# Optimization experiments

Measured on AMD Instinct MI355X. Metric: run time of the kernel, lower is better.

The kernel has to match this reference:

```python
import jax, jax.numpy as jnp
import numpy as np

NG, NC, FG, FC, D = 8192, 4096, 512, 256, 64
ALPHA = 0.2          # leaky_relu negative slope
NEG = -9.0e15        # mask fill value from the torch code


def _leaky(x):
    return jnp.where(x >= 0, x, ALPHA * x)


def _relation(h_src, h_dst, a, adj):
    # additive GAT score: e[i,j] = leaky(h_src[i]@a[:D] + h_dst[j]@a[D:])
    s1 = h_src @ a[:D]            # [Ns]
    s2 = h_dst @ a[D:]            # [Nd]
    e = _leaky(s1[:, None] + s2[None, :])          # [Ns, Nd]
    att = jax.nn.softmax(jnp.where(adj > 0, e, NEG), axis=1)
    return att @ h_dst            # [Ns, D]


def setup_inputs() -> dict:
    key = jax.random.key(0)
    ks = jax.random.split(key, 14)
    sc = 0.05
    return {
        "gene_x": jax.random.normal(ks[0], (NG, FG), jnp.float32),
        "cell_x": jax.random.normal(ks[1], (NC, FC), jnp.float32),
        "W_g": jax.random.normal(ks[2], (FG, D), jnp.float32) * sc,
        "W_c": jax.random.normal(ks[3], (FC, D), jnp.float32) * sc,
        "a_gg": jax.random.normal(ks[4], (2 * D,), jnp.float32) * sc,
        "a_gc": jax.random.normal(ks[5], (2 * D,), jnp.float32) * sc,
        "a_cc": jax.random.normal(ks[6], (2 * D,), jnp.float32) * sc,
        "a_cg": jax.random.normal(ks[7], (2 * D,), jnp.float32) * sc,
        "Wgate_g": jax.random.normal(ks[8], (D, 1), jnp.float32) * sc,
        "bgate_g": jnp.full((1,), -2.0, jnp.float32),
        "Wgate_c": jax.random.normal(ks[9], (D, 1), jnp.float32) * sc,
        "bgate_c": jnp.full((1,), -2.0, jnp.float32),
        "gene_adj": jax.random.randint(ks[10], (NG, NG), 0, 2, jnp.int32),
        "cell_adj": jax.random.randint(ks[11], (NC, NC), 0, 2, jnp.int32),
        "gene_cell_adj": jax.random.randint(ks[12], (NG, NC), 0, 2, jnp.int32),
    }


def reference(gene_x, cell_x, W_g, W_c, a_gg, a_gc, a_cc, a_cg,
              Wgate_g, bgate_g, Wgate_c, bgate_c,
              gene_adj, cell_adj, gene_cell_adj):
    gene_h = gene_x @ W_g                              # [NG, D]
    cell_h = cell_x @ W_c                              # [NC, D]

    gene_from_gene = _relation(gene_h, gene_h, a_gg, gene_adj)
    gene_from_cell = _relation(gene_h, cell_h, a_gc, gene_cell_adj)
    cell_from_cell = _relation(cell_h, cell_h, a_cc, cell_adj)
    cell_from_gene = _relation(cell_h, gene_h, a_cg, gene_cell_adj.T)

    gamma_g = jax.nn.sigmoid(gene_h @ Wgate_g + bgate_g)   # [NG, 1]
    gamma_c = jax.nn.sigmoid(cell_h @ Wgate_c + bgate_c)   # [NC, 1]

    gene_out = _leaky(gene_h + gene_from_gene + gamma_g * gene_from_cell)
    cell_out = _leaky(cell_h + cell_from_cell + gamma_c * cell_from_gene)
    return gene_out, cell_out
```

## Files before the change

### kernel.cpp

```cpp
#include <hip/hip_runtime.h>

#define NG 8192
#define NC 4096
#define FG 512
#define FC 256
#define ALPHA 0.2f

typedef float f32x4 __attribute__((ext_vector_type(4)));
typedef short bf16x8 __attribute__((ext_vector_type(8)));

static __device__ __forceinline__ float leakyf(float x) { return fmaxf(x, ALPHA * x); }

static __device__ __forceinline__ unsigned short f2bf(float f) {
    unsigned u = __builtin_bit_cast(unsigned, f);
    u += 0x7fffu + ((u >> 16) & 1u);
    return (unsigned short)(u >> 16);
}

static __device__ __forceinline__ float wred(float v) {
#pragma unroll
    for (int m = 1; m < 64; m <<= 1) v += __shfl_xor(v, m, 64);
    return v;
}

__global__ __launch_bounds__(256) void pack_all(
    const int* __restrict__ gene_adj, const int* __restrict__ cell_adj,
    const int* __restrict__ gc_adj,
    unsigned char* __restrict__ bmGG, unsigned char* __restrict__ bmCC,
    unsigned char* __restrict__ bmGC)
{
    const int wave = threadIdx.x >> 6, lane = threadIdx.x & 63;
    const int r = blockIdx.x * 4 + wave;
    const int* row; unsigned char* brow; int C;
    if (r < NG)           { row = gene_adj + (size_t)r * NG;              brow = bmGG + (size_t)r * (NG >> 3);              C = NG; }
    else if (r < NG + NC) { int rr = r - NG;      row = cell_adj + (size_t)rr * NC; brow = bmCC + (size_t)rr * (NC >> 3); C = NC; }
    else                  { int rr = r - NG - NC; row = gc_adj   + (size_t)rr * NC; brow = bmGC + (size_t)rr * (NC >> 3); C = NC; }
    for (int j = lane * 8; j < C; j += 512) {
        int4 a0 = *(const int4*)(row + j);
        int4 a1 = *(const int4*)(row + j + 4);
        unsigned b = (unsigned)(a0.x > 0)        | ((unsigned)(a0.y > 0) << 1)
                   | ((unsigned)(a0.z > 0) << 2) | ((unsigned)(a0.w > 0) << 3)
                   | ((unsigned)(a1.x > 0) << 4) | ((unsigned)(a1.y > 0) << 5)
                   | ((unsigned)(a1.z > 0) << 6) | ((unsigned)(a1.w > 0) << 7);
        brow[j >> 3] = (unsigned char)b;
    }
}

__global__ __launch_bounds__(256) void proj_kernel(
    const float* __restrict__ x, const float* __restrict__ W, int K, int N,
    float* __restrict__ h, unsigned short* __restrict__ hT,
    const float* __restrict__ aA, const float* __restrict__ aB,
    const float* __restrict__ aC, const float* __restrict__ aD,
    const float* __restrict__ aG, const float* __restrict__ bG,
    float* __restrict__ sA, float* __restrict__ sB, float* __restrict__ sC,
    float* __restrict__ sD, float* __restrict__ gam)
{
    const int wave = threadIdx.x >> 6, lane = threadIdx.x & 63;
    const int r0 = blockIdx.x * 16 + wave * 4;
    const float* xr = x + (size_t)r0 * K;
    float acc0 = 0.f, acc1 = 0.f, acc2 = 0.f, acc3 = 0.f;
    for (int k = 0; k < K; k += 4) {
        float4 x0 = *(const float4*)(xr + k);
        float4 x1 = *(const float4*)(xr + K + k);
        float4 x2 = *(const float4*)(xr + 2 * (size_t)K + k);
        float4 x3 = *(const float4*)(xr + 3 * (size_t)K + k);
        float w0 = W[(k + 0) * 64 + lane];
        float w1 = W[(k + 1) * 64 + lane];
        float w2 = W[(k + 2) * 64 + lane];
        float w3 = W[(k + 3) * 64 + lane];
        acc0 += x0.x * w0 + x0.y * w1 + x0.z * w2 + x0.w * w3;
        acc1 += x1.x * w0 + x1.y * w1 + x1.z * w2 + x1.w * w3;
        acc2 += x2.x * w0 + x2.y * w1 + x2.z * w2 + x2.w * w3;
        acc3 += x3.x * w0 + x3.y * w1 + x3.z * w2 + x3.w * w3;
    }
    float accs[4] = {acc0, acc1, acc2, acc3};
    unsigned short hb[4];
#pragma unroll
    for (int t = 0; t < 4; t++) {
        h[(size_t)(r0 + t) * 64 + lane] = accs[t];
        hb[t] = f2bf(accs[t]);
    }
    *(ushort4*)&hT[(size_t)lane * N + r0] = make_ushort4(hb[0], hb[1], hb[2], hb[3]);

    const float cA = aA[lane], cB = aB[lane], cC = aC[lane], cD = aD[lane], cG = aG[lane];
    const float bias = bG[0];
#pragma unroll
    for (int t = 0; t < 4; t++) {
        float vA = wred(accs[t] * cA);
        float vB = wred(accs[t] * cB);
        float vC = wred(accs[t] * cC);
        float vD = wred(accs[t] * cD);
        float vG = wred(accs[t] * cG);
        if (lane == 0) {
            sA[r0 + t] = vA; sB[r0 + t] = vB; sC[r0 + t] = vC; sD[r0 + t] = vD;
            gam[r0 + t] = 1.f / (1.f + __expf(-(vG + bias)));
        }
    }
}

static __device__ __forceinline__ void rel_row_body(
    unsigned short* hbuf,
    const unsigned char* __restrict__ bm, int bm_ld,
    const float* __restrict__ s1, const float* __restrict__ s2,
    const unsigned short* __restrict__ hT, int Nd,
    float* __restrict__ num, float* __restrict__ lsum, int Ns, int JS,
    int strip, int p)
{
    const int wave = threadIdx.x >> 6, lane = threadIdx.x & 63;
    const int m = lane & 15, kp = lane >> 4;
    const int jlen = Nd / JS, jbase = p * jlen;
    const int i_row = strip * 64 + wave * 16 + m;
    const float s1v = s1[i_row];
    const unsigned char* bmrow = bm + (size_t)i_row * bm_ld;
    f32x4 acc0 = {0.f, 0.f, 0.f, 0.f}, acc1 = acc0, acc2 = acc0, acc3 = acc0;
    float lacc = 0.f;

    for (int jc = jbase; jc < jbase + jlen; jc += 256) {
        uint4 q0 = *(const uint4*)(bmrow + (jc >> 3));
        uint4 q1 = *(const uint4*)(bmrow + (jc >> 3) + 16);
        for (int idx = threadIdx.x; idx < 2048; idx += 256) {
            int c = idx >> 5, off = (idx & 31) * 8;
            *(int4*)&hbuf[c * 264 + off] = *(const int4*)&hT[(size_t)c * Nd + jc + off];
        }
        __syncthreads();
        unsigned words[8] = {q0.x, q0.y, q0.z, q0.w, q1.x, q1.y, q1.z, q1.w};
#pragma unroll
        for (int g = 0; g < 8; ++g) {
            const int jg = jc + g * 32 + kp * 8;
            float4 sa = *(const float4*)&s2[jg];
            float4 sb = *(const float4*)&s2[jg + 4];
            unsigned byte = (words[g] >> (kp * 8)) & 0xffu;
            const int lb = g * 32 + kp * 8;
            bf16x8 b0 = *(const bf16x8*)&hbuf[(0 * 16 + m) * 264 + lb];
            bf16x8 b1 = *(const bf16x8*)&hbuf[(1 * 16 + m) * 264 + lb];
            bf16x8 b2 = *(const bf16x8*)&hbuf[(2 * 16 + m) * 264 + lb];
            bf16x8 b3 = *(const bf16x8*)&hbuf[(3 * 16 + m) * 264 + lb];
            float s2v[8] = {sa.x, sa.y, sa.z, sa.w, sb.x, sb.y, sb.z, sb.w};
            bf16x8 af;
#pragma unroll
            for (int t = 0; t < 8; t++) {
                float e = s1v + s2v[t];
                float w = ((byte >> t) & 1u) ? __expf(leakyf(e)) : 0.f;
                lacc += w;
                af[t] = (short)f2bf(w);
            }
            acc0 = __builtin_amdgcn_mfma_f32_16x16x32_bf16(af, b0, acc0, 0, 0, 0);
            acc1 = __builtin_amdgcn_mfma_f32_16x16x32_bf16(af, b1, acc1, 0, 0, 0);
            acc2 = __builtin_amdgcn_mfma_f32_16x16x32_bf16(af, b2, acc2, 0, 0, 0);
            acc3 = __builtin_amdgcn_mfma_f32_16x16x32_bf16(af, b3, acc3, 0, 0, 0);
        }
        __syncthreads();
    }
    const int orow0 = strip * 64 + wave * 16 + kp * 4;
#pragma unroll
    for (int r = 0; r < 4; r++) {
        size_t base = ((size_t)p * Ns + orow0 + r) * 64;
        num[base + m]      = acc0[r];
        num[base + 16 + m] = acc1[r];
        num[base + 32 + m] = acc2[r];
        num[base + 48 + m] = acc3[r];
    }
    lacc += __shfl_xor(lacc, 16, 64);
    lacc += __shfl_xor(lacc, 32, 64);
    if (kp == 0) lsum[(size_t)p * Ns + strip * 64 + wave * 16 + m] = lacc;
}

static __device__ __forceinline__ void rel_col_body(
    unsigned short* hbuf,
    unsigned char* bmb,
    const unsigned char* __restrict__ bm, int bm_ld,
    const float* __restrict__ s1, const float* __restrict__ s2,
    const unsigned short* __restrict__ hT, int Nd,
    float* __restrict__ num, float* __restrict__ lsum, int Ns, int JS,
    int strip, int p)
{
    const int wave = threadIdx.x >> 6, lane = threadIdx.x & 63;
    const int m = lane & 15, kp = lane >> 4;
    const int jlen = Nd / JS, jbase = p * jlen;
    const int i0 = strip * 64;
    const float s1v = s1[i0 + wave * 16 + m];
    f32x4 acc0 = {0.f, 0.f, 0.f, 0.f}, acc1 = acc0, acc2 = acc0, acc3 = acc0;
    float lacc = 0.f;
    const int bidx = wave * 2 + (m >> 3);
    const int bbit = m & 7;

    for (int jc = jbase; jc < jbase + jlen; jc += 128) {
        if (threadIdx.x < 128)
            *(unsigned long long*)&bmb[threadIdx.x * 8] =
                *(const unsigned long long*)&bm[(size_t)(jc + threadIdx.x) * bm_ld + (i0 >> 3)];
        for (int idx = threadIdx.x; idx < 1024; idx += 256) {
            int c = idx >> 4, off = (idx & 15) * 8;
            *(int4*)&hbuf[c * 136 + off] = *(const int4*)&hT[(size_t)c * Nd + jc + off];
        }
        __syncthreads();
#pragma unroll
        for (int g = 0; g < 4; ++g) {
            const int jg = jc + g * 32 + kp * 8;
            float4 sa = *(const float4*)&s2[jg];
            float4 sb = *(const float4*)&s2[jg + 4];
            const int jl = g * 32 + kp * 8;
            bf16x8 b0 = *(const bf16x8*)&hbuf[(0 * 16 + m) * 136 + jl];
            bf16x8 b1 = *(const bf16x8*)&hbuf[(1 * 16 + m) * 136 + jl];
            bf16x8 b2 = *(const bf16x8*)&hbuf[(2 * 16 + m) * 136 + jl];
            bf16x8 b3 = *(const bf16x8*)&hbuf[(3 * 16 + m) * 136 + jl];
            float s2v[8] = {sa.x, sa.y, sa.z, sa.w, sb.x, sb.y, sb.z, sb.w};
            bf16x8 af;
#pragma unroll
            for (int t = 0; t < 8; t++) {
                unsigned byte = bmb[(jl + t) * 8 + bidx];
                float e = s1v + s2v[t];
                float w = ((byte >> bbit) & 1u) ? __expf(leakyf(e)) : 0.f;
                lacc += w;
                af[t] = (short)f2bf(w);
            }
            acc0 = __builtin_amdgcn_mfma_f32_16x16x32_bf16(af, b0, acc0, 0, 0, 0);
            acc1 = __builtin_amdgcn_mfma_f32_16x16x32_bf16(af, b1, acc1, 0, 0, 0);
            acc2 = __builtin_amdgcn_mfma_f32_16x16x32_bf16(af, b2, acc2, 0, 0, 0);
            acc3 = __builtin_amdgcn_mfma_f32_16x16x32_bf16(af, b3, acc3, 0, 0, 0);
        }
        __syncthreads();
    }
    const int orow0 = strip * 64 + wave * 16 + kp * 4;
#pragma unroll
    for (int r = 0; r < 4; r++) {
        size_t base = ((size_t)p * Ns + orow0 + r) * 64;
        num[base + m]      = acc0[r];
        num[base + 16 + m] = acc1[r];
        num[base + 32 + m] = acc2[r];
        num[base + 48 + m] = acc3[r];
    }
    lacc += __shfl_xor(lacc, 16, 64);
    lacc += __shfl_xor(lacc, 32, 64);
    if (kp == 0) lsum[(size_t)p * Ns + strip * 64 + wave * 16 + m] = lacc;
}

__global__ __launch_bounds__(256, 4) void rel_fused(
    const unsigned char* __restrict__ bmGG, const unsigned char* __restrict__ bmCC,
    const unsigned char* __restrict__ bmGC,
    const float* __restrict__ s1gg, const float* __restrict__ s2gg,
    const float* __restrict__ s1cc, const float* __restrict__ s2cc,
    const float* __restrict__ s1gc, const float* __restrict__ s2gc,
    const float* __restrict__ s1cg, const float* __restrict__ s2cg,
    const unsigned short* __restrict__ gene_hT, const unsigned short* __restrict__ cell_hT,
    float* __restrict__ numGG, float* __restrict__ lGG,
    float* __restrict__ numCC, float* __restrict__ lCC,
    float* __restrict__ numGC, float* __restrict__ lGC,
    float* __restrict__ numCG, float* __restrict__ lCG)
{
    __shared__ __align__(16) char smem[64 * 264 * 2];
    const int b = blockIdx.x, rel = b >> 9, w = b & 511;
    if (rel == 0) {
        rel_row_body((unsigned short*)smem, bmGG, NG / 8, s1gg, s2gg, gene_hT, NG,
                     numGG, lGG, NG, 4, w >> 2, w & 3);
    } else if (rel == 1) {
        rel_row_body((unsigned short*)smem, bmCC, NC / 8, s1cc, s2cc, cell_hT, NC,
                     numCC, lCC, NC, 8, w >> 3, w & 7);
    } else if (rel == 2) {
        rel_row_body((unsigned short*)smem, bmGC, NC / 8, s1gc, s2gc, cell_hT, NC,
                     numGC, lGC, NG, 4, w >> 2, w & 3);
    } else {
        rel_col_body((unsigned short*)smem, (unsigned char*)(smem + 64 * 136 * 2),
                     bmGC, NC / 8, s1cg, s2cg, gene_hT, NG,
                     numCG, lCG, NC, 8, w >> 3, w & 7);
    }
}

__global__ __launch_bounds__(256) void combine_final(
    const float* __restrict__ numS, const float* __restrict__ lS, int JSS,
    const float* __restrict__ numX, const float* __restrict__ lX, int JSX,
    int Ns, const float* __restrict__ h, const float* __restrict__ gam,
    float* __restrict__ out)
{
    int idx = blockIdx.x * 256 + threadIdx.x;
    int i = idx >> 6, c = idx & 63;
    float nS = 0.f, dS = 0.f, nX = 0.f, dX = 0.f;
    for (int p = 0; p < JSS; p++) {
        nS += numS[((size_t)p * Ns + i) * 64 + c];
        dS += lS[(size_t)p * Ns + i];
    }
    for (int p = 0; p < JSX; p++) {
        nX += numX[((size_t)p * Ns + i) * 64 + c];
        dX += lX[(size_t)p * Ns + i];
    }
    float v = h[idx] + nS / dS + gam[i] * (nX / dX);
    out[idx] = leakyf(v);
}

extern "C" void kernel_launch(void* const* d_in, const int* in_sizes, int n_in,
                              void* d_out, int out_size, void* d_ws, size_t ws_size,
                              hipStream_t stream)
{
    const float* gene_x = (const float*)d_in[0];
    const float* cell_x = (const float*)d_in[1];
    const float* W_g    = (const float*)d_in[2];
    const float* W_c    = (const float*)d_in[3];
    const float* a_gg   = (const float*)d_in[4];
    const float* a_gc   = (const float*)d_in[5];
    const float* a_cc   = (const float*)d_in[6];
    const float* a_cg   = (const float*)d_in[7];
    const float* Wgg    = (const float*)d_in[8];
    const float* bgg    = (const float*)d_in[9];
    const float* Wgc    = (const float*)d_in[10];
    const float* bgc    = (const float*)d_in[11];
    const int* gene_adj = (const int*)d_in[12];
    const int* cell_adj = (const int*)d_in[13];
    const int* gc_adj   = (const int*)d_in[14];

    size_t off = 0;
    char* wsb = (char*)d_ws;
    auto alloc = [&](size_t bytes) -> void* {
        void* p = wsb + off;
        off += (bytes + 255) & ~(size_t)255;
        return p;
    };
    const int JS_GG = 4, JS_CC = 8, JS_GC = 4, JS_CG = 8;

    float* gene_h = (float*)alloc((size_t)NG * 64 * 4);
    float* cell_h = (float*)alloc((size_t)NC * 64 * 4);
    unsigned short* gene_hT = (unsigned short*)alloc((size_t)NG * 64 * 2);
    unsigned short* cell_hT = (unsigned short*)alloc((size_t)NC * 64 * 2);
    unsigned char* bmGG = (unsigned char*)alloc((size_t)NG * (NG / 8));
    unsigned char* bmCC = (unsigned char*)alloc((size_t)NC * (NC / 8));
    unsigned char* bmGC = (unsigned char*)alloc((size_t)NG * (NC / 8));
    float* s1gg = (float*)alloc(NG * 4);
    float* s2gg = (float*)alloc(NG * 4);
    float* s1gc = (float*)alloc(NG * 4);
    float* s2cg = (float*)alloc(NG * 4);
    float* gamg = (float*)alloc(NG * 4);
    float* s1cc = (float*)alloc(NC * 4);
    float* s2cc = (float*)alloc(NC * 4);
    float* s2gc = (float*)alloc(NC * 4);
    float* s1cg = (float*)alloc(NC * 4);
    float* gamc = (float*)alloc(NC * 4);
    float* numGG = (float*)alloc((size_t)NG * 64 * JS_GG * 4);
    float* lGG   = (float*)alloc((size_t)NG * JS_GG * 4);
    float* numGC = (float*)alloc((size_t)NG * 64 * JS_GC * 4);
    float* lGC   = (float*)alloc((size_t)NG * JS_GC * 4);
    float* numCC = (float*)alloc((size_t)NC * 64 * JS_CC * 4);
    float* lCC   = (float*)alloc((size_t)NC * JS_CC * 4);
    float* numCG = (float*)alloc((size_t)NC * 64 * JS_CG * 4);
    float* lCG   = (float*)alloc((size_t)NC * JS_CG * 4);

    float* out_gene = (float*)d_out;
    float* out_cell = (float*)d_out + (size_t)NG * 64;

    pack_all<<<(NG + NC + NG) / 4, 256, 0, stream>>>(gene_adj, cell_adj, gc_adj,
        bmGG, bmCC, bmGC);

    proj_kernel<<<NG / 16, 256, 0, stream>>>(gene_x, W_g, FG, NG, gene_h, gene_hT,
        a_gg, a_gg + 64, a_gc, a_cg + 64, Wgg, bgg, s1gg, s2gg, s1gc, s2cg, gamg);
    proj_kernel<<<NC / 16, 256, 0, stream>>>(cell_x, W_c, FC, NC, cell_h, cell_hT,
        a_cc, a_cc + 64, a_gc + 64, a_cg, Wgc, bgc, s1cc, s2cc, s2gc, s1cg, gamc);

    rel_fused<<<2048, 256, 0, stream>>>(bmGG, bmCC, bmGC,
        s1gg, s2gg, s1cc, s2cc, s1gc, s2gc, s1cg, s2cg,
        gene_hT, cell_hT,
        numGG, lGG, numCC, lCC, numGC, lGC, numCG, lCG);

    combine_final<<<NG * 64 / 256, 256, 0, stream>>>(numGG, lGG, JS_GG, numGC, lGC, JS_GC,
        NG, gene_h, gamg, out_gene);
    combine_final<<<NC * 64 / 256, 256, 0, stream>>>(numCC, lCC, JS_CC, numCG, lCG, JS_CG,
        NC, cell_h, gamc, out_cell);
}
```

Before: 692.4 us.

## Drop LDS staging in attention kernels, load hT directly; merge proj and combine launches

The relation kernels stop staging hT tiles and bitmask bytes through shared memory with block-wide barriers. Each lane now loads its bf16 B-fragments and mask bytes straight from global memory (L2/L1), which removes the __syncthreads and LDS traffic. The cost is more redundant global loads, plus strided single-byte mask reads in the column variant. The two projection launches and the two combine launches are each merged into one kernel to cut launch overhead.

```diff
diff --git a/kernel.cpp b/kernel.cpp
--- a/kernel.cpp
+++ b/kernel.cpp
@@ -46,17 +46,17 @@
     }
 }
 
-__global__ __launch_bounds__(256) void proj_kernel(
+static __device__ __forceinline__ void proj_body(
     const float* __restrict__ x, const float* __restrict__ W, int K, int N,
     float* __restrict__ h, unsigned short* __restrict__ hT,
     const float* __restrict__ aA, const float* __restrict__ aB,
     const float* __restrict__ aC, const float* __restrict__ aD,
     const float* __restrict__ aG, const float* __restrict__ bG,
     float* __restrict__ sA, float* __restrict__ sB, float* __restrict__ sC,
-    float* __restrict__ sD, float* __restrict__ gam)
+    float* __restrict__ sD, float* __restrict__ gam, int blk)
 {
     const int wave = threadIdx.x >> 6, lane = threadIdx.x & 63;
-    const int r0 = blockIdx.x * 16 + wave * 4;
+    const int r0 = blk * 16 + wave * 4;
     const float* xr = x + (size_t)r0 * K;
     float acc0 = 0.f, acc1 = 0.f, acc2 = 0.f, acc3 = 0.f;
     for (int k = 0; k < K; k += 4) {
@@ -98,8 +98,29 @@
     }
 }
 
-static __device__ __forceinline__ void rel_row_body(
-    unsigned short* hbuf,
+__global__ __launch_bounds__(256) void proj_all(
+    const float* __restrict__ gene_x, const float* __restrict__ W_g,
+    const float* __restrict__ cell_x, const float* __restrict__ W_c,
+    float* __restrict__ gene_h, unsigned short* __restrict__ gene_hT,
+    float* __restrict__ cell_h, unsigned short* __restrict__ cell_hT,
+    const float* __restrict__ a_gg, const float* __restrict__ a_gc,
+    const float* __restrict__ a_cc, const float* __restrict__ a_cg,
+    const float* __restrict__ Wgg, const float* __restrict__ bgg,
+    const float* __restrict__ Wgc, const float* __restrict__ bgc,
+    float* s1gg, float* s2gg, float* s1gc, float* s2cg, float* gamg,
+    float* s1cc, float* s2cc, float* s2gc, float* s1cg, float* gamc)
+{
+    if (blockIdx.x < NG / 16)
+        proj_body(gene_x, W_g, FG, NG, gene_h, gene_hT,
+                  a_gg, a_gg + 64, a_gc, a_cg + 64, Wgg, bgg,
+                  s1gg, s2gg, s1gc, s2cg, gamg, blockIdx.x);
+    else
+        proj_body(cell_x, W_c, FC, NC, cell_h, cell_hT,
+                  a_cc, a_cc + 64, a_gc + 64, a_cg, Wgc, bgc,
+                  s1cc, s2cc, s2gc, s1cg, gamc, blockIdx.x - NG / 16);
+}
+
+static __device__ __forceinline__ void rel_row_nb(
     const unsigned char* __restrict__ bm, int bm_ld,
     const float* __restrict__ s1, const float* __restrict__ s2,
     const unsigned short* __restrict__ hT, int Nd,
@@ -112,44 +133,36 @@
     const int i_row = strip * 64 + wave * 16 + m;
     const float s1v = s1[i_row];
     const unsigned char* bmrow = bm + (size_t)i_row * bm_ld;
+    const unsigned short* hb0 = hT + (size_t)(0 * 16 + m) * Nd;
+    const unsigned short* hb1 = hT + (size_t)(1 * 16 + m) * Nd;
+    const unsigned short* hb2 = hT + (size_t)(2 * 16 + m) * Nd;
+    const unsigned short* hb3 = hT + (size_t)(3 * 16 + m) * Nd;
     f32x4 acc0 = {0.f, 0.f, 0.f, 0.f}, acc1 = acc0, acc2 = acc0, acc3 = acc0;
     float lacc = 0.f;
-
-    for (int jc = jbase; jc < jbase + jlen; jc += 256) {
-        uint4 q0 = *(const uint4*)(bmrow + (jc >> 3));
-        uint4 q1 = *(const uint4*)(bmrow + (jc >> 3) + 16);
-        for (int idx = threadIdx.x; idx < 2048; idx += 256) {
-            int c = idx >> 5, off = (idx & 31) * 8;
-            *(int4*)&hbuf[c * 264 + off] = *(const int4*)&hT[(size_t)c * Nd + jc + off];
+    const int NGRP = jlen >> 5;
+#pragma unroll 2
+    for (int g = 0; g < NGRP; ++g) {
+        const int jg = jbase + g * 32 + kp * 8;
+        unsigned byte = bmrow[jg >> 3];
+        float4 sa = *(const float4*)&s2[jg];
+        float4 sb = *(const float4*)&s2[jg + 4];
+        bf16x8 b0 = *(const bf16x8*)&hb0[jg];
+        bf16x8 b1 = *(const bf16x8*)&hb1[jg];
+        bf16x8 b2 = *(const bf16x8*)&hb2[jg];
+        bf16x8 b3 = *(const bf16x8*)&hb3[jg];
+        float s2v[8] = {sa.x, sa.y, sa.z, sa.w, sb.x, sb.y, sb.z, sb.w};
+        bf16x8 af;
+#pragma unroll
+        for (int t = 0; t < 8; t++) {
+            float e = s1v + s2v[t];
+            float w = ((byte >> t) & 1u) ? __expf(leakyf(e)) : 0.f;
+            lacc += w;
+            af[t] = (short)f2bf(w);
         }
-        __syncthreads();
-        unsigned words[8] = {q0.x, q0.y, q0.z, q0.w, q1.x, q1.y, q1.z, q1.w};
-#pragma unroll
-        for (int g = 0; g < 8; ++g) {
-            const int jg = jc + g * 32 + kp * 8;
-            float4 sa = *(const float4*)&s2[jg];
-            float4 sb = *(const float4*)&s2[jg + 4];
-            unsigned byte = (words[g] >> (kp * 8)) & 0xffu;
-            const int lb = g * 32 + kp * 8;
-            bf16x8 b0 = *(const bf16x8*)&hbuf[(0 * 16 + m) * 264 + lb];
-            bf16x8 b1 = *(const bf16x8*)&hbuf[(1 * 16 + m) * 264 + lb];
-            bf16x8 b2 = *(const bf16x8*)&hbuf[(2 * 16 + m) * 264 + lb];
-            bf16x8 b3 = *(const bf16x8*)&hbuf[(3 * 16 + m) * 264 + lb];
-            float s2v[8] = {sa.x, sa.y, sa.z, sa.w, sb.x, sb.y, sb.z, sb.w};
-            bf16x8 af;
-#pragma unroll
-            for (int t = 0; t < 8; t++) {
-                float e = s1v + s2v[t];
-                float w = ((byte >> t) & 1u) ? __expf(leakyf(e)) : 0.f;
-                lacc += w;
-                af[t] = (short)f2bf(w);
-            }
-            acc0 = __builtin_amdgcn_mfma_f32_16x16x32_bf16(af, b0, acc0, 0, 0, 0);
-            acc1 = __builtin_amdgcn_mfma_f32_16x16x32_bf16(af, b1, acc1, 0, 0, 0);
-            acc2 = __builtin_amdgcn_mfma_f32_16x16x32_bf16(af, b2, acc2, 0, 0, 0);
-            acc3 = __builtin_amdgcn_mfma_f32_16x16x32_bf16(af, b3, acc3, 0, 0, 0);
-        }
-        __syncthreads();
+        acc0 = __builtin_amdgcn_mfma_f32_16x16x32_bf16(af, b0, acc0, 0, 0, 0);
+        acc1 = __builtin_amdgcn_mfma_f32_16x16x32_bf16(af, b1, acc1, 0, 0, 0);
+        acc2 = __builtin_amdgcn_mfma_f32_16x16x32_bf16(af, b2, acc2, 0, 0, 0);
+        acc3 = __builtin_amdgcn_mfma_f32_16x16x32_bf16(af, b3, acc3, 0, 0, 0);
     }
     const int orow0 = strip * 64 + wave * 16 + kp * 4;
 #pragma unroll
@@ -165,9 +178,7 @@
     if (kp == 0) lsum[(size_t)p * Ns + strip * 64 + wave * 16 + m] = lacc;
 }
 
-static __device__ __forceinline__ void rel_col_body(
-    unsigned short* hbuf,
-    unsigned char* bmb,
+static __device__ __forceinline__ void rel_col_nb(
     const unsigned char* __restrict__ bm, int bm_ld,
     const float* __restrict__ s1, const float* __restrict__ s2,
     const unsigned short* __restrict__ hT, int Nd,
@@ -177,48 +188,42 @@
     const int wave = threadIdx.x >> 6, lane = threadIdx.x & 63;
     const int m = lane & 15, kp = lane >> 4;
     const int jlen = Nd / JS, jbase = p * jlen;
-    const int i0 = strip * 64;
-    const float s1v = s1[i0 + wave * 16 + m];
+    const int i_row = strip * 64 + wave * 16 + m;
+    const float s1v = s1[i_row];
+    const int bcol = i_row >> 3, bbit = i_row & 7;
+    const unsigned short* hb0 = hT + (size_t)(0 * 16 + m) * Nd;
+    const unsigned short* hb1 = hT + (size_t)(1 * 16 + m) * Nd;
+    const unsigned short* hb2 = hT + (size_t)(2 * 16 + m) * Nd;
+    const unsigned short* hb3 = hT + (size_t)(3 * 16 + m) * Nd;
     f32x4 acc0 = {0.f, 0.f, 0.f, 0.f}, acc1 = acc0, acc2 = acc0, acc3 = acc0;
     float lacc = 0.f;
-    const int bidx = wave * 2 + (m >> 3);
-    const int bbit = m & 7;
-
-    for (int jc = jbase; jc < jbase + jlen; jc += 128) {
-        if (threadIdx.x < 128)
-            *(unsigned long long*)&bmb[threadIdx.x * 8] =
-                *(const unsigned long long*)&bm[(size_t)(jc + threadIdx.x) * bm_ld + (i0 >> 3)];
-        for (int idx = threadIdx.x; idx < 1024; idx += 256) {
-            int c = idx >> 4, off = (idx & 15) * 8;
-            *(int4*)&hbuf[c * 136 + off] = *(const int4*)&hT[(size_t)c * Nd + jc + off];
+    const int NGRP = jlen >> 5;
+#pragma unroll 2
+    for (int g = 0; g < NGRP; ++g) {
+        const int jg = jbase + g * 32 + kp * 8;
+        const unsigned char* bp = bm + (size_t)jg * bm_ld + bcol;
+        unsigned char by[8];
+#pragma unroll
+        for (int t = 0; t < 8; t++) by[t] = bp[(size_t)t * bm_ld];
+        float4 sa = *(const float4*)&s2[jg];
+        float4 sb = *(const float4*)&s2[jg + 4];
+        bf16x8 b0 = *(const bf16x8*)&hb0[jg];
+        bf16x8 b1 = *(const bf16x8*)&hb1[jg];
+        bf16x8 b2 = *(const bf16x8*)&hb2[jg];
+        bf16x8 b3 = *(const bf16x8*)&hb3[jg];
+        float s2v[8] = {sa.x, sa.y, sa.z, sa.w, sb.x, sb.y, sb.z, sb.w};
+        bf16x8 af;
+#pragma unroll
+        for (int t = 0; t < 8; t++) {
+            float e = s1v + s2v[t];
+            float w = ((by[t] >> bbit) & 1u) ? __expf(leakyf(e)) : 0.f;
+            lacc += w;
+            af[t] = (short)f2bf(w);
         }
-        __syncthreads();
-#pragma unroll
-        for (int g = 0; g < 4; ++g) {
-            const int jg = jc + g * 32 + kp * 8;
-            float4 sa = *(const float4*)&s2[jg];
-            float4 sb = *(const float4*)&s2[jg + 4];
-            const int jl = g * 32 + kp * 8;
-            bf16x8 b0 = *(const bf16x8*)&hbuf[(0 * 16 + m) * 136 + jl];
-            bf16x8 b1 = *(const bf16x8*)&hbuf[(1 * 16 + m) * 136 + jl];
-            bf16x8 b2 = *(const bf16x8*)&hbuf[(2 * 16 + m) * 136 + jl];
-            bf16x8 b3 = *(const bf16x8*)&hbuf[(3 * 16 + m) * 136 + jl];
-            float s2v[8] = {sa.x, sa.y, sa.z, sa.w, sb.x, sb.y, sb.z, sb.w};
-            bf16x8 af;
-#pragma unroll
-            for (int t = 0; t < 8; t++) {
-                unsigned byte = bmb[(jl + t) * 8 + bidx];
-                float e = s1v + s2v[t];
-                float w = ((byte >> bbit) & 1u) ? __expf(leakyf(e)) : 0.f;
-                lacc += w;
-                af[t] = (short)f2bf(w);
-            }
-            acc0 = __builtin_amdgcn_mfma_f32_16x16x32_bf16(af, b0, acc0, 0, 0, 0);
-            acc1 = __builtin_amdgcn_mfma_f32_16x16x32_bf16(af, b1, acc1, 0, 0, 0);
-            acc2 = __builtin_amdgcn_mfma_f32_16x16x32_bf16(af, b2, acc2, 0, 0, 0);
-            acc3 = __builtin_amdgcn_mfma_f32_16x16x32_bf16(af, b3, acc3, 0, 0, 0);
-        }
-        __syncthreads();
+        acc0 = __builtin_amdgcn_mfma_f32_16x16x32_bf16(af, b0, acc0, 0, 0, 0);
+        acc1 = __builtin_amdgcn_mfma_f32_16x16x32_bf16(af, b1, acc1, 0, 0, 0);
+        acc2 = __builtin_amdgcn_mfma_f32_16x16x32_bf16(af, b2, acc2, 0, 0, 0);
+        acc3 = __builtin_amdgcn_mfma_f32_16x16x32_bf16(af, b3, acc3, 0, 0, 0);
     }
     const int orow0 = strip * 64 + wave * 16 + kp * 4;
 #pragma unroll
@@ -247,31 +252,24 @@
     float* __restrict__ numGC, float* __restrict__ lGC,
     float* __restrict__ numCG, float* __restrict__ lCG)
 {
-    __shared__ __align__(16) char smem[64 * 264 * 2];
     const int b = blockIdx.x, rel = b >> 9, w = b & 511;
-    if (rel == 0) {
-        rel_row_body((unsigned short*)smem, bmGG, NG / 8, s1gg, s2gg, gene_hT, NG,
-                     numGG, lGG, NG, 4, w >> 2, w & 3);
-    } else if (rel == 1) {
-        rel_row_body((unsigned short*)smem, bmCC, NC / 8, s1cc, s2cc, cell_hT, NC,
-                     numCC, lCC, NC, 8, w >> 3, w & 7);
-    } else if (rel == 2) {
-        rel_row_body((unsigned short*)smem, bmGC, NC / 8, s1gc, s2gc, cell_hT, NC,
-                     numGC, lGC, NG, 4, w >> 2, w & 3);
-    } else {
-        rel_col_body((unsigned short*)smem, (unsigned char*)(smem + 64 * 136 * 2),
-                     bmGC, NC / 8, s1cg, s2cg, gene_hT, NG,
-                     numCG, lCG, NC, 8, w >> 3, w & 7);
-    }
-}
-
-__global__ __launch_bounds__(256) void combine_final(
+    if (rel == 0)
+        rel_row_nb(bmGG, NG / 8, s1gg, s2gg, gene_hT, NG, numGG, lGG, NG, 4, w >> 2, w & 3);
+    else if (rel == 1)
+        rel_row_nb(bmCC, NC / 8, s1cc, s2cc, cell_hT, NC, numCC, lCC, NC, 8, w >> 3, w & 7);
+    else if (rel == 2)
+        rel_row_nb(bmGC, NC / 8, s1gc, s2gc, cell_hT, NC, numGC, lGC, NG, 4, w >> 2, w & 3);
+    else
+        rel_col_nb(bmGC, NC / 8, s1cg, s2cg, gene_hT, NG, numCG, lCG, NC, 8, w >> 3, w & 7);
+}
+
+static __device__ __forceinline__ void combine_body(
     const float* __restrict__ numS, const float* __restrict__ lS, int JSS,
     const float* __restrict__ numX, const float* __restrict__ lX, int JSX,
     int Ns, const float* __restrict__ h, const float* __restrict__ gam,
-    float* __restrict__ out)
-{
-    int idx = blockIdx.x * 256 + threadIdx.x;
+    float* __restrict__ out, int blk)
+{
+    int idx = blk * 256 + threadIdx.x;
     int i = idx >> 6, c = idx & 63;
     float nS = 0.f, dS = 0.f, nX = 0.f, dX = 0.f;
     for (int p = 0; p < JSS; p++) {
@@ -284,6 +282,22 @@
     }
     float v = h[idx] + nS / dS + gam[i] * (nX / dX);
     out[idx] = leakyf(v);
+}
+
+__global__ __launch_bounds__(256) void combine_all(
+    const float* __restrict__ numGG, const float* __restrict__ lGG,
+    const float* __restrict__ numGC, const float* __restrict__ lGC,
+    const float* __restrict__ numCC, const float* __restrict__ lCC,
+    const float* __restrict__ numCG, const float* __restrict__ lCG,
+    const float* __restrict__ gene_h, const float* __restrict__ cell_h,
+    const float* __restrict__ gamg, const float* __restrict__ gamc,
+    float* __restrict__ out_gene, float* __restrict__ out_cell)
+{
+    if (blockIdx.x < NG * 64 / 256)
+        combine_body(numGG, lGG, 4, numGC, lGC, 4, NG, gene_h, gamg, out_gene, blockIdx.x);
+    else
+        combine_body(numCC, lCC, 8, numCG, lCG, 8, NC, cell_h, gamc, out_cell,
+                     blockIdx.x - NG * 64 / 256);
 }
 
 extern "C" void kernel_launch(void* const* d_in, const int* in_sizes, int n_in,
@@ -347,18 +361,17 @@
     pack_all<<<(NG + NC + NG) / 4, 256, 0, stream>>>(gene_adj, cell_adj, gc_adj,
         bmGG, bmCC, bmGC);
 
-    proj_kernel<<<NG / 16, 256, 0, stream>>>(gene_x, W_g, FG, NG, gene_h, gene_hT,
-        a_gg, a_gg + 64, a_gc, a_cg + 64, Wgg, bgg, s1gg, s2gg, s1gc, s2cg, gamg);
-    proj_kernel<<<NC / 16, 256, 0, stream>>>(cell_x, W_c, FC, NC, cell_h, cell_hT,
-        a_cc, a_cc + 64, a_gc + 64, a_cg, Wgc, bgc, s1cc, s2cc, s2gc, s1cg, gamc);
+    proj_all<<<NG / 16 + NC / 16, 256, 0, stream>>>(
+        gene_x, W_g, cell_x, W_c, gene_h, gene_hT, cell_h, cell_hT,
+        a_gg, a_gc, a_cc, a_cg, Wgg, bgg, Wgc, bgc,
+        s1gg, s2gg, s1gc, s2cg, gamg, s1cc, s2cc, s2gc, s1cg, gamc);
 
     rel_fused<<<2048, 256, 0, stream>>>(bmGG, bmCC, bmGC,
         s1gg, s2gg, s1cc, s2cc, s1gc, s2gc, s1cg, s2cg,
         gene_hT, cell_hT,
         numGG, lGG, numCC, lCC, numGC, lGC, numCG, lCG);
 
-    combine_final<<<NG * 64 / 256, 256, 0, stream>>>(numGG, lGG, JS_GG, numGC, lGC, JS_GC,
-        NG, gene_h, gamg, out_gene);
-    combine_final<<<NC * 64 / 256, 256, 0, stream>>>(numCC, lCC, JS_CC, numCG, lCG, JS_CG,
-        NC, cell_h, gamc, out_cell);
-}
+    combine_all<<<(NG + NC) * 64 / 256, 256, 0, stream>>>(
+        numGG, lGG, numGC, lGC, numCC, lCC, numCG, lCG,
+        gene_h, cell_h, gamg, gamc, out_gene, out_cell);
+}
```

Measured after the change: 743.0 us. 1.07x slower.
